# Kernel tuning notes

Measured on AMD Instinct MI355X. Metric: run time of the kernel, lower is better.

Reference implementation:

```python
import jax, jax.numpy as jnp
import numpy as np


def setup_inputs() -> dict:
    key = jax.random.key(0)
    B, D = 256, 4096
    continuous_input = jax.random.normal(key, (B, D), dtype=jnp.float32)
    return {"continuous_input": continuous_input, "timesteps": 100}


def reference(continuous_input, timesteps):
    # Temporal coding: each (batch, input) pair fires exactly one spike at a
    # time determined by sigmoid(value). With num_neurons == input_dim the
    # neuron index is just the input index, so the scalar scatter in the
    # original nested Python loops is exactly a one-hot over the time axis.
    T = timesteps
    # torch .long() truncates; sigmoid*(T-1) >= 0 so floor == trunc
    spike_times = jnp.floor(jax.nn.sigmoid(continuous_input) * (T - 1)).astype(jnp.int32)  # [B, D]
    t = jnp.arange(T, dtype=jnp.int32)  # [T]
    spikes = (t[:, None, None] == spike_times[None, :, :]).astype(jnp.float32)  # [T, B, N]
    return spikes
```

## Files before the change

kernel.cpp:

```cpp
#include <hip/hip_runtime.h>
#include <math.h>


typedef __attribute__((ext_vector_type(4))) float f32x4;

__device__ __forceinline__ float sigmoidf_(float x) {
    return 1.0f / (1.0f + expf(-x));
}

__global__ __launch_bounds__(256) void spike_time_kernel(
    const float* __restrict__ x, unsigned char* __restrict__ st,
    int n, float tm1) {
    const int e = (blockIdx.x * 256 + threadIdx.x) * 4;
    if (e + 3 < n) {
        f32x4 v = *reinterpret_cast<const f32x4*>(x + e);
        uchar4 s;
        s.x = (unsigned char)(int)(sigmoidf_(v.x) * tm1);
        s.y = (unsigned char)(int)(sigmoidf_(v.y) * tm1);
        s.z = (unsigned char)(int)(sigmoidf_(v.z) * tm1);
        s.w = (unsigned char)(int)(sigmoidf_(v.w) * tm1);
        *reinterpret_cast<uchar4*>(st + e) = s;
    } else {
        for (int i = e; i < n; ++i)
            st[i] = (unsigned char)(int)(sigmoidf_(x[i]) * tm1);
    }
}

__global__ __launch_bounds__(256) void write_onehot16_kernel(
    const unsigned char* __restrict__ st, float* __restrict__ out, int n) {
    const int t = blockIdx.y;
    const unsigned int tu = (unsigned int)t;
    const int e = (blockIdx.x * 256 + threadIdx.x) * 16;
    float* op = out + (size_t)t * n + e;
    if (e + 15 < n) {
        const uint4 s = *reinterpret_cast<const uint4*>(st + e);
        const unsigned int words[4] = {s.x, s.y, s.z, s.w};
#pragma unroll
        for (int w = 0; w < 4; ++w) {
            const unsigned int sw = words[w];
            f32x4 o;
            o.x = (((sw      ) & 0xffu) == tu) ? 1.0f : 0.0f;
            o.y = (((sw >>  8) & 0xffu) == tu) ? 1.0f : 0.0f;
            o.z = (((sw >> 16) & 0xffu) == tu) ? 1.0f : 0.0f;
            o.w = (((sw >> 24)        ) == tu) ? 1.0f : 0.0f;
            *(reinterpret_cast<f32x4*>(op) + w) = o;
        }
    } else {
        for (int i = e; i < n; ++i)
            out[(size_t)t * n + i] = (st[i] == (unsigned char)t) ? 1.0f : 0.0f;
    }
}

__global__ __launch_bounds__(256) void fused_onehot_kernel(
    const float* __restrict__ x, float* __restrict__ out, int n, float tm1) {
    const int t = blockIdx.y;
    const int e = (blockIdx.x * 256 + threadIdx.x) * 4;
    if (e + 3 < n) {
        f32x4 v = *reinterpret_cast<const f32x4*>(x + e);
        f32x4 o;
        o.x = ((int)(sigmoidf_(v.x) * tm1) == t) ? 1.0f : 0.0f;
        o.y = ((int)(sigmoidf_(v.y) * tm1) == t) ? 1.0f : 0.0f;
        o.z = ((int)(sigmoidf_(v.z) * tm1) == t) ? 1.0f : 0.0f;
        o.w = ((int)(sigmoidf_(v.w) * tm1) == t) ? 1.0f : 0.0f;
        *reinterpret_cast<f32x4*>(out + (size_t)t * n + e) = o;
    } else {
        for (int i = e; i < n; ++i)
            out[(size_t)t * n + i] = ((int)(sigmoidf_(x[i]) * tm1) == t) ? 1.0f : 0.0f;
    }
}

extern "C" void kernel_launch(void* const* d_in, const int* in_sizes, int n_in,
                              void* d_out, int out_size, void* d_ws, size_t ws_size,
                              hipStream_t stream) {
    const float* x = (const float*)d_in[0];
    float* out = (float*)d_out;
    const int n = in_sizes[0];
    const int T = out_size / n;
    const float tm1 = (float)(T - 1);

    const int n4 = (n + 3) / 4;
    const int blocks4 = (n4 + 255) / 256;

    if (ws_size >= (size_t)n && T <= 256) {
        unsigned char* st = (unsigned char*)d_ws;
        spike_time_kernel<<<blocks4, 256, 0, stream>>>(x, st, n, tm1);
        const int blocks16 = (n + 4095) / 4096;
        dim3 grid(blocks16, T);
        write_onehot16_kernel<<<grid, 256, 0, stream>>>(st, out, n);
    } else {
        dim3 grid(blocks4, T);
        fused_onehot_kernel<<<grid, 256, 0, stream>>>(x, out, n, tm1);
    }
}
```

Baseline: 452.7 us.

## Replace one-hot grid kernel with persistent chunked writer using prefetched spike times

Replaces the 2D grid one-hot writer, where each thread handles 16 elements, with a persistent-style kernel. About 1024 blocks each walk a contiguous range of 1024-float chunks, and each thread stores one float4 per chunk while prefetching the next spike-time word. The aim is to cut block launch overhead and keep write streams contiguous per block. In exchange each thread writes 16 bytes per iteration instead of 64, and the fast path now requires n to be a multiple of 1024.

After: 416.6 us. 1.09x faster.

```diff
diff --git a/kernel.cpp b/kernel.cpp
--- a/kernel.cpp
+++ b/kernel.cpp
@@ -6,6 +6,15 @@
 
 __device__ __forceinline__ float sigmoidf_(float x) {
     return 1.0f / (1.0f + expf(-x));
+}
+
+__device__ __forceinline__ f32x4 onehot4_(unsigned int sw, unsigned int tu) {
+    f32x4 o;
+    o.x = (((sw      ) & 0xffu) == tu) ? 1.0f : 0.0f;
+    o.y = (((sw >>  8) & 0xffu) == tu) ? 1.0f : 0.0f;
+    o.z = (((sw >> 16) & 0xffu) == tu) ? 1.0f : 0.0f;
+    o.w = (((sw >> 24)        ) == tu) ? 1.0f : 0.0f;
+    return o;
 }
 
 __global__ __launch_bounds__(256) void spike_time_kernel(
@@ -26,28 +35,34 @@
     }
 }
 
-__global__ __launch_bounds__(256) void write_onehot16_kernel(
-    const unsigned char* __restrict__ st, float* __restrict__ out, int n) {
-    const int t = blockIdx.y;
-    const unsigned int tu = (unsigned int)t;
-    const int e = (blockIdx.x * 256 + threadIdx.x) * 16;
-    float* op = out + (size_t)t * n + e;
-    if (e + 15 < n) {
-        const uint4 s = *reinterpret_cast<const uint4*>(st + e);
-        const unsigned int words[4] = {s.x, s.y, s.z, s.w};
-#pragma unroll
-        for (int w = 0; w < 4; ++w) {
-            const unsigned int sw = words[w];
-            f32x4 o;
-            o.x = (((sw      ) & 0xffu) == tu) ? 1.0f : 0.0f;
-            o.y = (((sw >>  8) & 0xffu) == tu) ? 1.0f : 0.0f;
-            o.z = (((sw >> 16) & 0xffu) == tu) ? 1.0f : 0.0f;
-            o.w = (((sw >> 24)        ) == tu) ? 1.0f : 0.0f;
-            *(reinterpret_cast<f32x4*>(op) + w) = o;
-        }
-    } else {
-        for (int i = e; i < n; ++i)
-            out[(size_t)t * n + i] = (st[i] == (unsigned char)t) ? 1.0f : 0.0f;
+__global__ __launch_bounds__(256) void write_onehot_persist_kernel(
+    const unsigned char* __restrict__ st, float* __restrict__ out,
+    int n, int total_chunks, int cpb) {
+    const int cpp = n >> 10;
+    const int c0 = blockIdx.x * cpb;
+    int cend = c0 + cpb;
+    if (cend > total_chunks) cend = total_chunks;
+    if (c0 >= cend) return;
+
+    const int lane4 = threadIdx.x * 4;
+    int t  = c0 / cpp;
+    int lc = c0 - t * cpp;
+
+    unsigned int s_next =
+        *reinterpret_cast<const unsigned int*>(st + (lc << 10) + lane4);
+    float* op = out + (size_t)c0 * 1024 + lane4;
+
+    for (int c = c0; c < cend; ++c) {
+        const unsigned int s_cur = s_next;
+        const unsigned int tu = (unsigned int)t;
+        int lc_n = lc + 1, t_n = t;
+        if (lc_n == cpp) { lc_n = 0; ++t_n; }
+        if (c + 1 < cend)
+            s_next = *reinterpret_cast<const unsigned int*>(
+                st + (lc_n << 10) + lane4);
+        *reinterpret_cast<f32x4*>(op) = onehot4_(s_cur, tu);
+        op += 1024;
+        lc = lc_n; t = t_n;
     }
 }
 
@@ -81,12 +96,15 @@
     const int n4 = (n + 3) / 4;
     const int blocks4 = (n4 + 255) / 256;
 
-    if (ws_size >= (size_t)n && T <= 256) {
+    if (ws_size >= (size_t)n && T <= 256 && (n & 1023) == 0) {
         unsigned char* st = (unsigned char*)d_ws;
         spike_time_kernel<<<blocks4, 256, 0, stream>>>(x, st, n, tm1);
-        const int blocks16 = (n + 4095) / 4096;
-        dim3 grid(blocks16, T);
-        write_onehot16_kernel<<<grid, 256, 0, stream>>>(st, out, n);
+        const int total_chunks = (int)(((size_t)T * n) >> 10);
+        const int target_blocks = 1024;
+        const int cpb = (total_chunks + target_blocks - 1) / target_blocks;
+        const int blocks = (total_chunks + cpb - 1) / cpb;
+        write_onehot_persist_kernel<<<blocks, 256, 0, stream>>>(
+            st, out, n, total_chunks, cpb);
     } else {
         dim3 grid(blocks4, T);
         fused_onehot_kernel<<<grid, 256, 0, stream>>>(x, out, n, tm1);
```

## Replace per-timestep grid with persistent blocks looping over timesteps

Applied to the files above, without the earlier changes.

The one-hot writer now launches one block per 4096-element group and loops over all timesteps inside the kernel. Each thread loads its spike-time bytes once and keeps them in registers, then writes four strided float4 chunks per timestep. This removes the repeated spike-time reads and the block scheduling cost of a T-sized grid. The cost is far fewer blocks and waves in flight, which may limit store throughput. The path also now requires n to be a multiple of 4096.

Result: faster. 407.4 us (-10.0%).

```diff
diff --git a/kernel.cpp b/kernel.cpp
--- a/kernel.cpp
+++ b/kernel.cpp
@@ -6,6 +6,15 @@
 
 __device__ __forceinline__ float sigmoidf_(float x) {
     return 1.0f / (1.0f + expf(-x));
+}
+
+__device__ __forceinline__ f32x4 onehot4_(unsigned int sw, unsigned int tu) {
+    f32x4 o;
+    o.x = (((sw      ) & 0xffu) == tu) ? 1.0f : 0.0f;
+    o.y = (((sw >>  8) & 0xffu) == tu) ? 1.0f : 0.0f;
+    o.z = (((sw >> 16) & 0xffu) == tu) ? 1.0f : 0.0f;
+    o.w = (((sw >> 24)        ) == tu) ? 1.0f : 0.0f;
+    return o;
 }
 
 __global__ __launch_bounds__(256) void spike_time_kernel(
@@ -26,28 +35,29 @@
     }
 }
 
-__global__ __launch_bounds__(256) void write_onehot16_kernel(
-    const unsigned char* __restrict__ st, float* __restrict__ out, int n) {
-    const int t = blockIdx.y;
-    const unsigned int tu = (unsigned int)t;
-    const int e = (blockIdx.x * 256 + threadIdx.x) * 16;
-    float* op = out + (size_t)t * n + e;
-    if (e + 15 < n) {
-        const uint4 s = *reinterpret_cast<const uint4*>(st + e);
-        const unsigned int words[4] = {s.x, s.y, s.z, s.w};
-#pragma unroll
-        for (int w = 0; w < 4; ++w) {
-            const unsigned int sw = words[w];
-            f32x4 o;
-            o.x = (((sw      ) & 0xffu) == tu) ? 1.0f : 0.0f;
-            o.y = (((sw >>  8) & 0xffu) == tu) ? 1.0f : 0.0f;
-            o.z = (((sw >> 16) & 0xffu) == tu) ? 1.0f : 0.0f;
-            o.w = (((sw >> 24)        ) == tu) ? 1.0f : 0.0f;
-            *(reinterpret_cast<f32x4*>(op) + w) = o;
-        }
-    } else {
-        for (int i = e; i < n; ++i)
-            out[(size_t)t * n + i] = (st[i] == (unsigned char)t) ? 1.0f : 0.0f;
+__global__ __launch_bounds__(256) void write_onehot_gs_kernel(
+    const unsigned char* __restrict__ st, float* __restrict__ out,
+    int G, int nk) {
+    const int b = blockIdx.x;
+    const int lane4 = threadIdx.x * 4;
+    const unsigned int s0 = *reinterpret_cast<const unsigned int*>(
+        st + ((size_t)b << 10) + lane4);
+    const unsigned int s1 = *reinterpret_cast<const unsigned int*>(
+        st + ((size_t)(b + G) << 10) + lane4);
+    const unsigned int s2 = *reinterpret_cast<const unsigned int*>(
+        st + ((size_t)(b + 2 * G) << 10) + lane4);
+    const unsigned int s3 = *reinterpret_cast<const unsigned int*>(
+        st + ((size_t)(b + 3 * G) << 10) + lane4);
+
+    const size_t step = (size_t)G << 10;
+    float* op = out + ((size_t)b << 10) + lane4;
+    for (int k = 0; k < nk; k += 4) {
+        const unsigned int tu = (unsigned int)(k >> 2);
+        *reinterpret_cast<f32x4*>(op)            = onehot4_(s0, tu);
+        *reinterpret_cast<f32x4*>(op + step)     = onehot4_(s1, tu);
+        *reinterpret_cast<f32x4*>(op + 2 * step) = onehot4_(s2, tu);
+        *reinterpret_cast<f32x4*>(op + 3 * step) = onehot4_(s3, tu);
+        op += 4 * step;
     }
 }
 
@@ -81,12 +91,12 @@
     const int n4 = (n + 3) / 4;
     const int blocks4 = (n4 + 255) / 256;
 
-    if (ws_size >= (size_t)n && T <= 256) {
+    if (ws_size >= (size_t)n && T <= 256 && (n & 4095) == 0) {
         unsigned char* st = (unsigned char*)d_ws;
         spike_time_kernel<<<blocks4, 256, 0, stream>>>(x, st, n, tm1);
-        const int blocks16 = (n + 4095) / 4096;
-        dim3 grid(blocks16, T);
-        write_onehot16_kernel<<<grid, 256, 0, stream>>>(st, out, n);
+        const int G = n >> 12;
+        const int nk = 4 * T;
+        write_onehot_gs_kernel<<<G, 256, 0, stream>>>(st, out, G, nk);
     } else {
         dim3 grid(blocks4, T);
         fused_onehot_kernel<<<grid, 256, 0, stream>>>(x, out, n, tm1);
```
